# Kernel tuning notes

Measured on AMD Instinct MI355X. Metric: run time of the kernel, lower is better.

The kernel has to match this reference:

```python
import jax, jax.numpy as jnp
import numpy as np

B, L, XS, YS, A, C, NL = 32, 4096, 256, 256, 4, 64, 5  # batch, seq, x_size, y_size, n_actions, hid_cnn, cnn_layers


def _conv2d(x, w):
    # x: [N,Cin,H,W], w: [Cout,Cin,3,3], stride 1, pad 1 ('SAME')
    return jax.lax.conv_general_dilated(x, w, (1, 1), 'SAME',
                                        dimension_numbers=('NCHW', 'OIHW', 'NCHW'))


def setup_inputs() -> dict:
    key = jax.random.key(0)
    ks = jax.random.split(key, 16)
    stdv = 1.0 / np.sqrt(XS)
    inp = {
        'x': jax.random.normal(ks[0], (B, L, XS), jnp.float32),
        'y': jax.random.normal(ks[1], (B, YS), jnp.float32),
        'x_mask': jax.random.randint(ks[2], (B, L), 0, 2) == 1,
        'actions': jax.random.randint(ks[3], (B,), 0, A),
        'weight': jax.random.uniform(ks[4], (YS, XS), jnp.float32, -stdv, stdv),
    }
    chans = [(1, C)] + [(C, C)] * (NL - 2) + [(C, 1)]
    for i, (ci, co) in enumerate(chans):
        bound = 1.0 / np.sqrt(ci * 9)
        inp[f'cw{i}'] = jax.random.uniform(ks[5 + 2 * i], (A, co, ci, 3, 3), jnp.float32, -bound, bound)
        inp[f'cb{i}'] = jax.random.uniform(ks[6 + 2 * i], (A, co), jnp.float32, -bound, bound)
    return inp


def reference(x, y, x_mask, actions, weight,
              cw0, cb0, cw1, cb1, cw2, cb2, cw3, cb3, cw4, cb4):
    img = weight[None, None]  # [1,1,YS,XS] -- weight matrix as a 1-channel image

    def per_action(w0, b0, w1, b1, w2, b2, w3, b3, w4, b4):
        out = img
        layers = ((w0, b0), (w1, b1), (w2, b2), (w3, b3), (w4, b4))
        for i, (w, b) in enumerate(layers):
            out = _conv2d(out, w) + b[None, :, None, None]
            if i < NL - 1:
                out = jax.nn.relu(out)
        return out[0, 0]  # [YS,XS]

    # all per-action conv stacks batched via vmap -> [A,YS,XS]
    W_a = jax.vmap(per_action)(cw0, cb0, cw1, cb1, cw2, cb2, cw3, cb3, cw4, cb4)
    # one-hot multiply + sum over actions == select the per-sample action matrix
    Wy = jnp.einsum('bh,bhx->bx', y, W_a[actions])          # [B,XS]
    xWy = jnp.einsum('blx,bx->bl', x, Wy)                   # [B,L]
    xWy = jnp.where(x_mask, -jnp.inf, xWy)
    return jax.nn.softmax(xWy, axis=-1)  # eval-mode output (training uses log_softmax)
```

## Files before the change

### kernel.cpp

```cpp
#include <hip/hip_runtime.h>
#include <cstdint>
#include <cstddef>

typedef __attribute__((ext_vector_type(8))) short bf16x8;
typedef __attribute__((ext_vector_type(4))) float f32x4;
typedef __attribute__((ext_vector_type(4))) int i32x4;

__device__ inline unsigned short cvt_bf16_rne(float f) {
    unsigned u = __builtin_bit_cast(unsigned, f);
    u = (u + 0x7FFFu + ((u >> 16) & 1u)) >> 16;
    return (unsigned short)u;
}
__device__ inline float bf16_to_f32(unsigned short s) {
    return __builtin_bit_cast(float, (unsigned)s << 16);
}

__global__ void clear_flag_kernel(int* flag) {
    if (threadIdx.x == 0) *flag = 0;
}

__global__ void detect_mask_kernel(const unsigned int* m, int* flag) {
    int i = blockIdx.x * blockDim.x + threadIdx.x;
    int f = 0;
    #pragma unroll
    for (int k = 0; k < 4; ++k) {
        unsigned int v = m[i * 4 + k];
        if (v == 0x3F800000u) f |= 2;
        else if (v > 1u) f |= 1;
    }
    if (f) atomicOr(flag, f);
}

__global__ void apack_kernel(const float* __restrict__ cw, char* __restrict__ apack) {
    int t = threadIdx.x;
    int tap = blockIdx.x, a = blockIdx.y;
    int ks = t >> 8, mf = (t >> 6) & 3, lane = t & 63;
    int n = lane & 15, q = lane >> 4;
    int co = mf * 16 + n;
    int ci0 = ks * 32 + q * 8;
    unsigned d[4];
    #pragma unroll
    for (int jj = 0; jj < 4; ++jj) {
        unsigned short h0 = cvt_bf16_rne(cw[((size_t)(a * 64 + co) * 64 + ci0 + 2 * jj + 0) * 9 + tap]);
        unsigned short h1 = cvt_bf16_rne(cw[((size_t)(a * 64 + co) * 64 + ci0 + 2 * jj + 1) * 9 + tap]);
        d[jj] = (unsigned)h0 | ((unsigned)h1 << 16);
    }
    *(i32x4*)(apack + ((((size_t)(a * 9 + tap) * 2 + ks) * 4 + mf) * 1024 + lane * 16)) =
        *(i32x4*)d;
}

__global__ void conv_first_kernel(const float* __restrict__ img,
                                  const float* __restrict__ cw0,
                                  const float* __restrict__ cb0,
                                  unsigned short* __restrict__ act) {
    int y = blockIdx.x, a = blockIdx.y, x = threadIdx.x;
    float p[3][3];
    #pragma unroll
    for (int ty = 0; ty < 3; ++ty)
        #pragma unroll
        for (int tx = 0; tx < 3; ++tx) {
            int py = y + ty - 1, px = x + tx - 1;
            p[ty][tx] = ((unsigned)py < 256u && (unsigned)px < 256u)
                        ? img[py * 256 + px] : 0.0f;
        }
    const float* w = cw0 + (size_t)a * 64 * 9;
    const float* b = cb0 + a * 64;
    unsigned pk[32];
    #pragma unroll
    for (int co = 0; co < 64; ++co) {
        const float* wc = w + co * 9;
        float acc = b[co];
        #pragma unroll
        for (int ty = 0; ty < 3; ++ty)
            #pragma unroll
            for (int tx = 0; tx < 3; ++tx)
                acc = fmaf(wc[ty * 3 + tx], p[ty][tx], acc);
        acc = fmaxf(acc, 0.0f);
        unsigned short hv = cvt_bf16_rne(acc);
        if (co & 1) pk[co >> 1] |= ((unsigned)hv << 16);
        else        pk[co >> 1] = (unsigned)hv;
    }
    char* ob = (char*)act + (((size_t)(a << 16) + (y << 8) + x) << 7);
    #pragma unroll
    for (int k = 0; k < 8; ++k)
        *(i32x4*)(ob + k * 16) = *(i32x4*)&pk[k * 4];
}

__global__ __launch_bounds__(256, 3)
void conv_mid_mfma(const unsigned short* __restrict__ act_in,
                   const char* __restrict__ apack_l,
                   const float* __restrict__ cb,
                   unsigned short* __restrict__ act_out) {
    __shared__ i32x4 lds4[340 * 9];
    int tid = threadIdx.x;
    int a = blockIdx.z;
    int r0 = blockIdx.y * 8, c0 = blockIdx.x * 32;
    const char* actb = (const char*)act_in;

    for (int s = tid; s < 2720; s += 256) {
        int px = s >> 3, o = s & 7;
        int prow = px / 34, pcol = px - prow * 34;
        int grow = r0 - 1 + prow, gcol = c0 - 1 + pcol;
        i32x4 v = {0, 0, 0, 0};
        if ((unsigned)grow < 256u && (unsigned)gcol < 256u)
            v = *(const i32x4*)(actb + (((size_t)(a << 16) + (grow << 8) + gcol) << 7) + (o << 4));
        lds4[px * 9 + o] = v;
    }
    __syncthreads();

    int lane = tid & 63, wv = tid >> 6;
    int n = lane & 15, q = lane >> 4;

    f32x4 acc[4][4];
    #pragma unroll
    for (int mf = 0; mf < 4; ++mf) {
        f32x4 bb = *(const f32x4*)(cb + a * 64 + mf * 16 + q * 4);
        #pragma unroll
        for (int nf = 0; nf < 4; ++nf) acc[mf][nf] = bb;
    }

    int base_nf[4];
    #pragma unroll
    for (int nf = 0; nf < 4; ++nf) {
        int orl = wv * 2 + (nf >> 1);
        int ocl = ((nf & 1) << 4) + n;
        base_nf[nf] = (orl * 34 + ocl) * 9 + q;
    }
    const char* ap = apack_l + (size_t)a * 9 * 8192 + lane * 16;

    #pragma unroll
    for (int tap = 0; tap < 9; ++tap) {
        const int ty = tap / 3, tx = tap - ty * 3;
        const int toff = (ty * 34 + tx) * 9;
        #pragma unroll
        for (int ks = 0; ks < 2; ++ks) {
            bf16x8 Af[4], Bf[4];
            #pragma unroll
            for (int mf = 0; mf < 4; ++mf)
                Af[mf] = __builtin_bit_cast(bf16x8,
                    *(const i32x4*)(ap + (((tap * 2 + ks) * 4 + mf) << 10)));
            #pragma unroll
            for (int nf = 0; nf < 4; ++nf)
                Bf[nf] = __builtin_bit_cast(bf16x8, lds4[base_nf[nf] + toff + ks * 4]);
            #pragma unroll
            for (int mf = 0; mf < 4; ++mf)
                #pragma unroll
                for (int nf = 0; nf < 4; ++nf)
                    acc[mf][nf] = __builtin_amdgcn_mfma_f32_16x16x32_bf16(
                        Af[mf], Bf[nf], acc[mf][nf], 0, 0, 0);
        }
    }

    #pragma unroll
    for (int nf = 0; nf < 4; ++nf) {
        int grow = r0 + wv * 2 + (nf >> 1);
        int gcol = c0 + ((nf & 1) << 4) + n;
        char* ob = (char*)act_out + (((size_t)(a << 16) + (grow << 8) + gcol) << 7) + q * 8;
        #pragma unroll
        for (int mf = 0; mf < 4; ++mf) {
            f32x4 v = acc[mf][nf];
            unsigned d0 = (unsigned)cvt_bf16_rne(fmaxf(v.x, 0.0f))
                        | ((unsigned)cvt_bf16_rne(fmaxf(v.y, 0.0f)) << 16);
            unsigned d1 = (unsigned)cvt_bf16_rne(fmaxf(v.z, 0.0f))
                        | ((unsigned)cvt_bf16_rne(fmaxf(v.w, 0.0f)) << 16);
            uint2 st; st.x = d0; st.y = d1;
            *(uint2*)(ob + mf * 32) = st;
        }
    }
}

__global__ void conv_last_kernel(const unsigned short* __restrict__ act,
                                 const float* __restrict__ cw4,
                                 const float* __restrict__ cb4,
                                 float* __restrict__ W_a) {
    int y = blockIdx.x, a = blockIdx.y;
    int tid = threadIdx.x;
    int lane = tid & 63, wv = tid >> 6;
    int o = lane & 7, pl = lane >> 3;
    float wr[8][9];
    #pragma unroll
    for (int j = 0; j < 8; ++j) {
        const float* wp = cw4 + ((size_t)a * 64 + o * 8 + j) * 9;
        #pragma unroll
        for (int t = 0; t < 9; ++t) wr[j][t] = wp[t];
    }
    const char* actb = (const char*)act;
    float bias = cb4[a];
    for (int i = 0; i < 8; ++i) {
        int x = i * 32 + wv * 8 + pl;
        float p = 0.0f;
        #pragma unroll
        for (int ty = 0; ty < 3; ++ty) {
            int py = y + ty - 1;
            #pragma unroll
            for (int tx = 0; tx < 3; ++tx) {
                int px = x + tx - 1;
                if ((unsigned)py < 256u && (unsigned)px < 256u) {
                    i32x4 v = *(const i32x4*)(actb +
                        (((size_t)(a << 16) + (py << 8) + px) << 7) + (o << 4));
                    const unsigned* dv = (const unsigned*)&v;
                    #pragma unroll
                    for (int j = 0; j < 8; ++j) {
                        unsigned d = dv[j >> 1];
                        unsigned short us = (j & 1) ? (unsigned short)(d >> 16)
                                                    : (unsigned short)(d & 0xffffu);
                        p = fmaf(bf16_to_f32(us), wr[j][ty * 3 + tx], p);
                    }
                }
            }
        }
        p += __shfl_xor(p, 1, 64);
        p += __shfl_xor(p, 2, 64);
        p += __shfl_xor(p, 4, 64);
        if (o == 0) W_a[(size_t)(a << 16) + (y << 8) + x] = p + bias;
    }
}

__global__ void wy_kernel(const float* __restrict__ yv,
                          const int* __restrict__ actions,
                          const float* __restrict__ W_a,
                          float* __restrict__ Wy) {
    int b = blockIdx.x, x = threadIdx.x;
    int a = actions[b];
    const float* Wp = W_a + (size_t)a * 65536;
    const float* yb = yv + b * 256;
    float acc = 0.0f;
    #pragma unroll 8
    for (int h = 0; h < 256; ++h)
        acc = fmaf(yb[h], Wp[(size_t)h * 256 + x], acc);
    Wy[b * 256 + x] = acc;
}

__global__ void logits_kernel(const float* __restrict__ xv,
                              const void* __restrict__ mask,
                              const int* __restrict__ flag,
                              const float* __restrict__ Wy,
                              float* __restrict__ out) {
    int tid = threadIdx.x, lane = tid & 63, wave = tid >> 6;
    int b = blockIdx.y;
    int fl = *flag;
    float4 wy4 = *(const float4*)(Wy + b * 256 + lane * 4);
    const float* xb = xv + (size_t)b * 4096 * 256;
    int l0 = blockIdx.x * 128 + wave * 32;
    for (int li = 0; li < 32; ++li) {
        int l = l0 + li;
        const float4 x4 = *(const float4*)(xb + (size_t)l * 256 + lane * 4);
        float p = x4.x * wy4.x + x4.y * wy4.y + x4.z * wy4.z + x4.w * wy4.w;
        #pragma unroll
        for (int off = 32; off > 0; off >>= 1)
            p += __shfl_xor(p, off, 64);
        if (lane == 0) {
            size_t mi = (size_t)b * 4096 + l;
            bool msk;
            if (fl & 2)      msk = ((const float*)mask)[mi] != 0.0f;
            else if (fl & 1) msk = ((const unsigned char*)mask)[mi] != 0;
            else             msk = ((const int*)mask)[mi] != 0;
            out[mi] = msk ? -__builtin_inff() : p;
        }
    }
}

__global__ void softmax_kernel(float* __restrict__ out) {
    int b = blockIdx.x, tid = threadIdx.x;
    int lane = tid & 63, wid = tid >> 6;
    float* row = out + (size_t)b * 4096;
    float v[4];
    float m = -__builtin_inff();
    #pragma unroll
    for (int i = 0; i < 4; ++i) { v[i] = row[tid + i * 1024]; m = fmaxf(m, v[i]); }
    #pragma unroll
    for (int off = 32; off > 0; off >>= 1) m = fmaxf(m, __shfl_xor(m, off, 64));
    __shared__ float redm[16];
    __shared__ float reds[16];
    if (lane == 0) redm[wid] = m;
    __syncthreads();
    float M = redm[0];
    #pragma unroll
    for (int j = 1; j < 16; ++j) M = fmaxf(M, redm[j]);
    float s = 0.0f;
    #pragma unroll
    for (int i = 0; i < 4; ++i) { v[i] = expf(v[i] - M); s += v[i]; }
    #pragma unroll
    for (int off = 32; off > 0; off >>= 1) s += __shfl_xor(s, off, 64);
    if (lane == 0) reds[wid] = s;
    __syncthreads();
    float S = 0.0f;
    #pragma unroll
    for (int j = 0; j < 16; ++j) S += reds[j];
    float inv = 1.0f / S;
    #pragma unroll
    for (int i = 0; i < 4; ++i) row[tid + i * 1024] = v[i] * inv;
}

extern "C" void kernel_launch(void* const* d_in, const int* in_sizes, int n_in,
                              void* d_out, int out_size, void* d_ws, size_t ws_size,
                              hipStream_t stream) {
    const float* xv      = (const float*)d_in[0];
    const float* yv      = (const float*)d_in[1];
    const void*  xmask   = d_in[2];
    const int*   actions = (const int*)d_in[3];
    const float* weight  = (const float*)d_in[4];
    const float* cw0 = (const float*)d_in[5];
    const float* cb0 = (const float*)d_in[6];
    const float* cw1 = (const float*)d_in[7];
    const float* cb1 = (const float*)d_in[8];
    const float* cw2 = (const float*)d_in[9];
    const float* cb2 = (const float*)d_in[10];
    const float* cw3 = (const float*)d_in[11];
    const float* cb3 = (const float*)d_in[12];
    const float* cw4 = (const float*)d_in[13];
    const float* cb4 = (const float*)d_in[14];
    float* out = (float*)d_out;

    char* ws = (char*)d_ws;
    unsigned short* bufA = (unsigned short*)ws;
    unsigned short* bufB = (unsigned short*)(ws + 33554432);
    char*  apack = ws + 67108864;
    float* W_a   = (float*)(ws + 67993600);
    float* Wy    = (float*)(ws + 69042176);
    int*   flag  = (int*)(ws + 69074944);

    clear_flag_kernel<<<1, 64, 0, stream>>>(flag);
    detect_mask_kernel<<<32, 256, 0, stream>>>((const unsigned int*)xmask, flag);

    apack_kernel<<<dim3(9, 4), 512, 0, stream>>>(cw1, apack);
    apack_kernel<<<dim3(9, 4), 512, 0, stream>>>(cw2, apack + 294912);
    apack_kernel<<<dim3(9, 4), 512, 0, stream>>>(cw3, apack + 589824);

    conv_first_kernel<<<dim3(256, 4), 256, 0, stream>>>(weight, cw0, cb0, bufA);
    conv_mid_mfma<<<dim3(8, 32, 4), 256, 0, stream>>>(bufA, apack,          cb1, bufB);
    conv_mid_mfma<<<dim3(8, 32, 4), 256, 0, stream>>>(bufB, apack + 294912, cb2, bufA);
    conv_mid_mfma<<<dim3(8, 32, 4), 256, 0, stream>>>(bufA, apack + 589824, cb3, bufB);
    conv_last_kernel<<<dim3(256, 4), 256, 0, stream>>>(bufB, cw4, cb4, W_a);

    wy_kernel<<<32, 256, 0, stream>>>(yv, actions, W_a, Wy);
    logits_kernel<<<dim3(32, 32), 256, 0, stream>>>(xv, xmask, flag, Wy, out);
    softmax_kernel<<<32, 1024, 0, stream>>>(out);
}
```

Before: 403.1 us.

## Fuse prep kernels and retile mid convs with planar LDS layout

Merges mask detection, weight packing and the first conv into a single prep launch, which removes several small kernel launches. The mid-layer MFMA conv tile shrinks from 32 to 16 columns, giving twice as many blocks and lower register and LDS use, with launch bounds raised to 4 blocks per CU. The LDS layout changes to channel-group planes with padding, presumably to cut bank conflicts. The last conv also unpacks bf16 pairs more cheaply; the cost is a larger halo overhead per output pixel in the smaller tiles.

```diff
diff --git a/kernel.cpp b/kernel.cpp
--- a/kernel.cpp
+++ b/kernel.cpp
@@ -5,156 +5,166 @@
 typedef __attribute__((ext_vector_type(8))) short bf16x8;
 typedef __attribute__((ext_vector_type(4))) float f32x4;
 typedef __attribute__((ext_vector_type(4))) int i32x4;
+
+#define HALO_W   18
+#define PLANEPAD 181
 
 __device__ inline unsigned short cvt_bf16_rne(float f) {
     unsigned u = __builtin_bit_cast(unsigned, f);
     u = (u + 0x7FFFu + ((u >> 16) & 1u)) >> 16;
     return (unsigned short)u;
 }
-__device__ inline float bf16_to_f32(unsigned short s) {
-    return __builtin_bit_cast(float, (unsigned)s << 16);
-}
-
-__global__ void clear_flag_kernel(int* flag) {
-    if (threadIdx.x == 0) *flag = 0;
-}
-
-__global__ void detect_mask_kernel(const unsigned int* m, int* flag) {
-    int i = blockIdx.x * blockDim.x + threadIdx.x;
+
+__global__ void prep_kernel(const float* __restrict__ img,
+                            const float* __restrict__ cw0,
+                            const float* __restrict__ cb0,
+                            unsigned short* __restrict__ act,
+                            const float* __restrict__ cw1,
+                            const float* __restrict__ cw2,
+                            const float* __restrict__ cw3,
+                            char* __restrict__ apack,
+                            const unsigned int* __restrict__ mask,
+                            int* __restrict__ flag) {
+    int bid = blockIdx.x, tid = threadIdx.x;
+
+    if (bid < 1024) {
+        int y = bid & 255, a = bid >> 8, x = tid;
+        float p[3][3];
+        #pragma unroll
+        for (int ty = 0; ty < 3; ++ty)
+            #pragma unroll
+            for (int tx = 0; tx < 3; ++tx) {
+                int py = y + ty - 1, px = x + tx - 1;
+                p[ty][tx] = ((unsigned)py < 256u && (unsigned)px < 256u)
+                            ? img[py * 256 + px] : 0.0f;
+            }
+        const float* w = cw0 + (size_t)a * 64 * 9;
+        const float* b = cb0 + a * 64;
+        unsigned pk[32];
+        #pragma unroll
+        for (int co = 0; co < 64; ++co) {
+            const float* wc = w + co * 9;
+            float acc = b[co];
+            #pragma unroll
+            for (int ty = 0; ty < 3; ++ty)
+                #pragma unroll
+                for (int tx = 0; tx < 3; ++tx)
+                    acc = fmaf(wc[ty * 3 + tx], p[ty][tx], acc);
+            acc = fmaxf(acc, 0.0f);
+            unsigned short hv = cvt_bf16_rne(acc);
+            if (co & 1) pk[co >> 1] |= ((unsigned)hv << 16);
+            else        pk[co >> 1] = (unsigned)hv;
+        }
+        char* ob = (char*)act + (((size_t)(a << 16) + (y << 8) + x) << 7);
+        #pragma unroll
+        for (int k = 0; k < 8; ++k)
+            *(i32x4*)(ob + k * 16) = *(i32x4*)&pk[k * 4];
+        return;
+    }
+
+    if (bid < 1240) {
+        int idx = (bid - 1024) * 256 + tid;
+        int layer = idx / 18432;
+        int r = idx - layer * 18432;
+        int lane = r & 63, mf = (r >> 6) & 3;
+        int t = r >> 8;
+        int tap = t % 9, t2 = t / 9;
+        int ks = t2 & 1, a = t2 >> 1;
+        int n = lane & 15, q = lane >> 4;
+        int co = mf * 16 + n;
+        int ci0 = ks * 32 + q * 8;
+        const float* cw = (layer == 0) ? cw1 : (layer == 1) ? cw2 : cw3;
+        unsigned d[4];
+        #pragma unroll
+        for (int jj = 0; jj < 4; ++jj) {
+            unsigned short h0 = cvt_bf16_rne(cw[((size_t)(a * 64 + co) * 64 + ci0 + 2 * jj + 0) * 9 + tap]);
+            unsigned short h1 = cvt_bf16_rne(cw[((size_t)(a * 64 + co) * 64 + ci0 + 2 * jj + 1) * 9 + tap]);
+            d[jj] = (unsigned)h0 | ((unsigned)h1 << 16);
+        }
+        *(i32x4*)(apack + (size_t)idx * 16) = *(i32x4*)d;
+        return;
+    }
+
+    __shared__ int red;
+    if (tid == 0) red = 0;
+    __syncthreads();
     int f = 0;
-    #pragma unroll
-    for (int k = 0; k < 4; ++k) {
-        unsigned int v = m[i * 4 + k];
+    for (int k = 0; k < 128; ++k) {
+        unsigned v = mask[k * 256 + tid];
         if (v == 0x3F800000u) f |= 2;
         else if (v > 1u) f |= 1;
     }
-    if (f) atomicOr(flag, f);
-}
-
-__global__ void apack_kernel(const float* __restrict__ cw, char* __restrict__ apack) {
-    int t = threadIdx.x;
-    int tap = blockIdx.x, a = blockIdx.y;
-    int ks = t >> 8, mf = (t >> 6) & 3, lane = t & 63;
-    int n = lane & 15, q = lane >> 4;
-    int co = mf * 16 + n;
-    int ci0 = ks * 32 + q * 8;
-    unsigned d[4];
-    #pragma unroll
-    for (int jj = 0; jj < 4; ++jj) {
-        unsigned short h0 = cvt_bf16_rne(cw[((size_t)(a * 64 + co) * 64 + ci0 + 2 * jj + 0) * 9 + tap]);
-        unsigned short h1 = cvt_bf16_rne(cw[((size_t)(a * 64 + co) * 64 + ci0 + 2 * jj + 1) * 9 + tap]);
-        d[jj] = (unsigned)h0 | ((unsigned)h1 << 16);
-    }
-    *(i32x4*)(apack + ((((size_t)(a * 9 + tap) * 2 + ks) * 4 + mf) * 1024 + lane * 16)) =
-        *(i32x4*)d;
-}
-
-__global__ void conv_first_kernel(const float* __restrict__ img,
-                                  const float* __restrict__ cw0,
-                                  const float* __restrict__ cb0,
-                                  unsigned short* __restrict__ act) {
-    int y = blockIdx.x, a = blockIdx.y, x = threadIdx.x;
-    float p[3][3];
-    #pragma unroll
-    for (int ty = 0; ty < 3; ++ty)
-        #pragma unroll
-        for (int tx = 0; tx < 3; ++tx) {
-            int py = y + ty - 1, px = x + tx - 1;
-            p[ty][tx] = ((unsigned)py < 256u && (unsigned)px < 256u)
-                        ? img[py * 256 + px] : 0.0f;
-        }
-    const float* w = cw0 + (size_t)a * 64 * 9;
-    const float* b = cb0 + a * 64;
-    unsigned pk[32];
-    #pragma unroll
-    for (int co = 0; co < 64; ++co) {
-        const float* wc = w + co * 9;
-        float acc = b[co];
-        #pragma unroll
-        for (int ty = 0; ty < 3; ++ty)
-            #pragma unroll
-            for (int tx = 0; tx < 3; ++tx)
-                acc = fmaf(wc[ty * 3 + tx], p[ty][tx], acc);
-        acc = fmaxf(acc, 0.0f);
-        unsigned short hv = cvt_bf16_rne(acc);
-        if (co & 1) pk[co >> 1] |= ((unsigned)hv << 16);
-        else        pk[co >> 1] = (unsigned)hv;
-    }
-    char* ob = (char*)act + (((size_t)(a << 16) + (y << 8) + x) << 7);
-    #pragma unroll
-    for (int k = 0; k < 8; ++k)
-        *(i32x4*)(ob + k * 16) = *(i32x4*)&pk[k * 4];
-}
-
-__global__ __launch_bounds__(256, 3)
+    if (f) atomicOr(&red, f);
+    __syncthreads();
+    if (tid == 0) *flag = red;
+}
+
+__global__ __launch_bounds__(256, 4)
 void conv_mid_mfma(const unsigned short* __restrict__ act_in,
                    const char* __restrict__ apack_l,
                    const float* __restrict__ cb,
                    unsigned short* __restrict__ act_out) {
-    __shared__ i32x4 lds4[340 * 9];
+    __shared__ i32x4 lds4[8 * PLANEPAD];
     int tid = threadIdx.x;
     int a = blockIdx.z;
-    int r0 = blockIdx.y * 8, c0 = blockIdx.x * 32;
+    int r0 = blockIdx.y * 8, c0 = blockIdx.x * 16;
     const char* actb = (const char*)act_in;
 
-    for (int s = tid; s < 2720; s += 256) {
-        int px = s >> 3, o = s & 7;
-        int prow = px / 34, pcol = px - prow * 34;
+    for (int s = tid; s < 1448; s += 256) {
+        int o = s & 7, px = s >> 3;
+        int prow = px / HALO_W;
+        int pcol = px - prow * HALO_W;
         int grow = r0 - 1 + prow, gcol = c0 - 1 + pcol;
         i32x4 v = {0, 0, 0, 0};
         if ((unsigned)grow < 256u && (unsigned)gcol < 256u)
             v = *(const i32x4*)(actb + (((size_t)(a << 16) + (grow << 8) + gcol) << 7) + (o << 4));
-        lds4[px * 9 + o] = v;
+        lds4[o * PLANEPAD + px] = v;
     }
     __syncthreads();
 
     int lane = tid & 63, wv = tid >> 6;
     int n = lane & 15, q = lane >> 4;
 
-    f32x4 acc[4][4];
+    f32x4 acc[4][2];
     #pragma unroll
     for (int mf = 0; mf < 4; ++mf) {
         f32x4 bb = *(const f32x4*)(cb + a * 64 + mf * 16 + q * 4);
-        #pragma unroll
-        for (int nf = 0; nf < 4; ++nf) acc[mf][nf] = bb;
-    }
-
-    int base_nf[4];
-    #pragma unroll
-    for (int nf = 0; nf < 4; ++nf) {
-        int orl = wv * 2 + (nf >> 1);
-        int ocl = ((nf & 1) << 4) + n;
-        base_nf[nf] = (orl * 34 + ocl) * 9 + q;
-    }
-    const char* ap = apack_l + (size_t)a * 9 * 8192 + lane * 16;
-
-    #pragma unroll
-    for (int tap = 0; tap < 9; ++tap) {
-        const int ty = tap / 3, tx = tap - ty * 3;
-        const int toff = (ty * 34 + tx) * 9;
-        #pragma unroll
-        for (int ks = 0; ks < 2; ++ks) {
-            bf16x8 Af[4], Bf[4];
+        acc[mf][0] = bb;
+        acc[mf][1] = bb;
+    }
+
+    const char* ap = apack_l + (size_t)a * 73728 + lane * 16;
+
+    #pragma unroll
+    for (int ks = 0; ks < 2; ++ks) {
+        const char* apk = ap + ks * 36864;
+        int pbase = (ks * 4 + q) * PLANEPAD;
+        #pragma unroll
+        for (int tap = 0; tap < 9; ++tap) {
+            const int ty = tap / 3, tx = tap - ty * 3;
+            bf16x8 Af[4], Bf[2];
             #pragma unroll
             for (int mf = 0; mf < 4; ++mf)
                 Af[mf] = __builtin_bit_cast(bf16x8,
-                    *(const i32x4*)(ap + (((tap * 2 + ks) * 4 + mf) << 10)));
-            #pragma unroll
-            for (int nf = 0; nf < 4; ++nf)
-                Bf[nf] = __builtin_bit_cast(bf16x8, lds4[base_nf[nf] + toff + ks * 4]);
+                    *(const i32x4*)(apk + tap * 4096 + mf * 1024));
+            #pragma unroll
+            for (int nf = 0; nf < 2; ++nf) {
+                int px = (wv * 2 + nf + ty) * HALO_W + n + tx;
+                Bf[nf] = __builtin_bit_cast(bf16x8, lds4[pbase + px]);
+            }
             #pragma unroll
             for (int mf = 0; mf < 4; ++mf)
                 #pragma unroll
-                for (int nf = 0; nf < 4; ++nf)
+                for (int nf = 0; nf < 2; ++nf)
                     acc[mf][nf] = __builtin_amdgcn_mfma_f32_16x16x32_bf16(
                         Af[mf], Bf[nf], acc[mf][nf], 0, 0, 0);
         }
     }
 
     #pragma unroll
-    for (int nf = 0; nf < 4; ++nf) {
-        int grow = r0 + wv * 2 + (nf >> 1);
-        int gcol = c0 + ((nf & 1) << 4) + n;
+    for (int nf = 0; nf < 2; ++nf) {
+        int grow = r0 + wv * 2 + nf;
+        int gcol = c0 + n;
         char* ob = (char*)act_out + (((size_t)(a << 16) + (grow << 8) + gcol) << 7) + q * 8;
         #pragma unroll
         for (int mf = 0; mf < 4; ++mf) {
@@ -200,11 +210,12 @@
                         (((size_t)(a << 16) + (py << 8) + px) << 7) + (o << 4));
                     const unsigned* dv = (const unsigned*)&v;
                     #pragma unroll
-                    for (int j = 0; j < 8; ++j) {
-                        unsigned d = dv[j >> 1];
-                        unsigned short us = (j & 1) ? (unsigned short)(d >> 16)
-                                                    : (unsigned short)(d & 0xffffu);
-                        p = fmaf(bf16_to_f32(us), wr[j][ty * 3 + tx], p);
+                    for (int k = 0; k < 4; ++k) {
+                        unsigned d = dv[k];
+                        float flo = __builtin_bit_cast(float, d << 16);
+                        float fhi = __builtin_bit_cast(float, d & 0xFFFF0000u);
+                        p = fmaf(flo, wr[2 * k + 0][ty * 3 + tx], p);
+                        p = fmaf(fhi, wr[2 * k + 1][ty * 3 + tx], p);
                     }
                 }
             }
@@ -320,17 +331,13 @@
     float* Wy    = (float*)(ws + 69042176);
     int*   flag  = (int*)(ws + 69074944);
 
-    clear_flag_kernel<<<1, 64, 0, stream>>>(flag);
-    detect_mask_kernel<<<32, 256, 0, stream>>>((const unsigned int*)xmask, flag);
-
-    apack_kernel<<<dim3(9, 4), 512, 0, stream>>>(cw1, apack);
-    apack_kernel<<<dim3(9, 4), 512, 0, stream>>>(cw2, apack + 294912);
-    apack_kernel<<<dim3(9, 4), 512, 0, stream>>>(cw3, apack + 589824);
-
-    conv_first_kernel<<<dim3(256, 4), 256, 0, stream>>>(weight, cw0, cb0, bufA);
-    conv_mid_mfma<<<dim3(8, 32, 4), 256, 0, stream>>>(bufA, apack,          cb1, bufB);
-    conv_mid_mfma<<<dim3(8, 32, 4), 256, 0, stream>>>(bufB, apack + 294912, cb2, bufA);
-    conv_mid_mfma<<<dim3(8, 32, 4), 256, 0, stream>>>(bufA, apack + 589824, cb3, bufB);
+    prep_kernel<<<1241, 256, 0, stream>>>(weight, cw0, cb0, bufA,
+                                          cw1, cw2, cw3, apack,
+                                          (const unsigned int*)xmask, flag);
+
+    conv_mid_mfma<<<dim3(16, 32, 4), 256, 0, stream>>>(bufA, apack,          cb1, bufB);
+    conv_mid_mfma<<<dim3(16, 32, 4), 256, 0, stream>>>(bufB, apack + 294912, cb2, bufA);
+    conv_mid_mfma<<<dim3(16, 32, 4), 256, 0, stream>>>(bufA, apack + 589824, cb3, bufB);
     conv_last_kernel<<<dim3(256, 4), 256, 0, stream>>>(bufB, cw4, cb4, W_a);
 
     wy_kernel<<<32, 256, 0, stream>>>(yv, actions, W_a, Wy);
```

Measured after the change: 437.0 us. 1.08x slower.
